# Kernel optimization log

Measured on AMD Instinct MI355X. Metric: run time of the kernel, lower is better.

The kernel has to match this reference:

```python
import jax, jax.numpy as jnp
import numpy as np

B, C, H_LEVELS = 262144, 128, 4
LEVEL_SIZES = [8, 24, 40, 56]  # partitions the C classes across hierarchy levels
ALPHA_BCE = 1.0
ALPHA_LAM = 0.5
LOG_CLAMP = -100.0  # torch F.binary_cross_entropy clamps log terms at -100


def setup_inputs() -> dict:
    key = jax.random.key(0)
    k1, k2 = jax.random.split(key)
    y_pred = jax.random.normal(k1, (B, C), dtype=jnp.float32)
    y_true = jnp.round(jax.random.uniform(k2, (B, C), dtype=jnp.float32))  # binary labels
    # La[l, c] = 1 if class c belongs to hierarchy level l (contiguous blocks)
    La = np.zeros((H_LEVELS, C), dtype=np.float32)
    off = 0
    for l, s in enumerate(LEVEL_SIZES):
        La[l, off:off + s] = 1.0
        off += s
    La = jnp.asarray(La)
    hc = jnp.arange(H_LEVELS, 0, -1).astype(jnp.float32)  # [h, h-1, ..., 1]
    lam = jnp.exp(-ALPHA_LAM * hc)
    return {"y_pred": y_pred, "y_true": y_true, "La": La, "lam": lam}


def reference(y_pred, y_true, La, lam):
    # alpha_c = alpha_d = alpha_e = 0, so only the layered-BCE term contributes.
    p = jax.nn.sigmoid(y_pred)                 # [B, C]
    pm = p[:, None, :] * La[None, :, :]        # [B, h, C] masked probs
    tm = y_true[:, None, :] * La[None, :, :]   # [B, h, C] masked targets
    log_p = jnp.clip(jnp.log(pm), LOG_CLAMP)
    log_1mp = jnp.clip(jnp.log1p(-pm), LOG_CLAMP)
    bce = -(tm * log_p + (1.0 - tm) * log_1mp)  # [B, h, C]
    per_layer = bce.mean(axis=2)                # [B, h] (mean reduction over C)
    # sum over layers weighted by lam, then sum over batch (original does NOT divide by B)
    bce_loss = jnp.sum(per_layer * lam[None, :])
    return ALPHA_BCE * bce_loss
```

## Files before the change

### kernel.cpp

```cpp
#include <hip/hip_runtime.h>

#define NCLS 128
#define HLVL 4
#define BLOCKS 8192
#define CHUNK 1024

typedef float v4f __attribute__((ext_vector_type(4)));

__global__ void prep_kernel(const float* __restrict__ La,
                            const float* __restrict__ lam,
                            float* __restrict__ w) {
    int c = threadIdx.x;
    if (c < NCLS) {
        float acc = 0.f;
#pragma unroll
        for (int l = 0; l < HLVL; ++l) acc += La[l * NCLS + c] * lam[l];
        w[c] = acc * (1.0f / (float)NCLS);
    }
}

__global__ __launch_bounds__(256) void loss_kernel(const v4f* __restrict__ yp,
                                                   const v4f* __restrict__ yt,
                                                   const float* __restrict__ w,
                                                   float* __restrict__ partial) {
    const float LOG2E = 1.44269504088896340736f;
    const float LN2   = 0.69314718055994530942f;

    int t = threadIdx.x;
    int b = blockIdx.x * CHUNK + t;
    int cbase = (t * 4) & (NCLS - 1);
    v4f w4 = *(const v4f*)(w + cbase);
    float wv[4] = {w4.x, w4.y, w4.z, w4.w};
    float wl[4] = {w4.x * LN2, w4.y * LN2, w4.z * LN2, w4.w * LN2};

    v4f x[4], y[4];
#pragma unroll
    for (int k = 0; k < 4; ++k) {
        x[k] = yp[b + k * 256];
        y[k] = yt[b + k * 256];
    }

    float acc[4] = {0.f, 0.f, 0.f, 0.f};
#pragma unroll
    for (int k = 0; k < 4; ++k) {
        float xs[4] = {x[k].x, x[k].y, x[k].z, x[k].w};
        float ts[4] = {y[k].x, y[k].y, y[k].z, y[k].w};
#pragma unroll
        for (int j = 0; j < 4; ++j) {
            float xv = xs[j];
            float e  = __builtin_amdgcn_exp2f(-fabsf(xv) * LOG2E);
            float l2 = __builtin_amdgcn_logf(1.0f + e);
            float r  = fmaf(-ts[j], xv, fmaxf(xv, 0.f));
            acc[j] = fmaf(l2, wl[j], acc[j]);
            acc[j] = fmaf(r, wv[j], acc[j]);
        }
    }
    float a = (acc[0] + acc[1]) + (acc[2] + acc[3]);

#pragma unroll
    for (int off = 32; off > 0; off >>= 1)
        a += __shfl_down(a, off, 64);

    __shared__ float bsum[4];
    if ((t & 63) == 0) bsum[t >> 6] = a;
    __syncthreads();
    if (t == 0)
        partial[blockIdx.x] = (bsum[0] + bsum[1]) + (bsum[2] + bsum[3]);
}

__global__ __launch_bounds__(256) void final_kernel(const float* __restrict__ partial,
                                                    float* __restrict__ out) {
    int t = threadIdx.x;
    float a = 0.f;
#pragma unroll
    for (int k = 0; k < BLOCKS / 256; ++k)
        a += partial[t + k * 256];
#pragma unroll
    for (int off = 32; off > 0; off >>= 1)
        a += __shfl_down(a, off, 64);
    __shared__ float bsum[4];
    if ((t & 63) == 0) bsum[t >> 6] = a;
    __syncthreads();
    if (t == 0)
        out[0] = (bsum[0] + bsum[1]) + (bsum[2] + bsum[3]);
}

extern "C" void kernel_launch(void* const* d_in, const int* in_sizes, int n_in,
                              void* d_out, int out_size, void* d_ws, size_t ws_size,
                              hipStream_t stream) {
    const float* y_pred = (const float*)d_in[0];
    const float* y_true = (const float*)d_in[1];
    const float* La     = (const float*)d_in[2];
    const float* lam    = (const float*)d_in[3];
    float* out = (float*)d_out;
    float* w       = (float*)d_ws;
    float* partial = (float*)d_ws + NCLS;

    prep_kernel<<<1, 128, 0, stream>>>(La, lam, w);

    loss_kernel<<<BLOCKS, 256, 0, stream>>>((const v4f*)y_pred,
                                            (const v4f*)y_true,
                                            w, partial);

    final_kernel<<<1, 256, 0, stream>>>(partial, out);
}
```

Baseline: 279.3 us.

## Double-buffer loss inputs through LDS with async global_load_lds pipelining

The loss kernel now has each block process a larger batch chunk in stages. Each stage's inputs are staged into a double-buffered LDS array with global_load_lds, and the next stage's copy is issued before computing on the current one. A hand-encoded s_waitcnt on vmcnt waits for the right loads. The aim is to keep more memory traffic in flight per wave and hide HBM latency, while using four times fewer blocks. In exchange the hand-written waitcnt encoding adds correctness risk and there is no lgkm wait guarding buffer reuse, and fewer blocks mean less parallelism across the GPU.

```diff
diff --git a/kernel.cpp b/kernel.cpp
--- a/kernel.cpp
+++ b/kernel.cpp
@@ -2,10 +2,15 @@
 
 #define NCLS 128
 #define HLVL 4
-#define BLOCKS 8192
-#define CHUNK 1024
+#define BLOCKS 2048
+#define BCHUNK 4096
+#define STAGE 512
+#define NSTAGE (BCHUNK / STAGE)
 
-typedef float v4f __attribute__((ext_vector_type(4)));
+typedef const __attribute__((address_space(1))) void* gas_t;
+typedef __attribute__((address_space(3))) void* las_t;
+
+#define WCNT(n) __builtin_amdgcn_s_waitcnt(((n) & 15) | 0x70 | 0xF00 | (((n) >> 4) << 14))
 
 __global__ void prep_kernel(const float* __restrict__ La,
                             const float* __restrict__ lam,
@@ -19,41 +24,61 @@
     }
 }
 
-__global__ __launch_bounds__(256) void loss_kernel(const v4f* __restrict__ yp,
-                                                   const v4f* __restrict__ yt,
+__global__ __launch_bounds__(256) void loss_kernel(const float4* __restrict__ yp,
+                                                   const float4* __restrict__ yt,
                                                    const float* __restrict__ w,
                                                    float* __restrict__ partial) {
+    __shared__ float4 lds[2][2][STAGE];
     const float LOG2E = 1.44269504088896340736f;
     const float LN2   = 0.69314718055994530942f;
 
     int t = threadIdx.x;
-    int b = blockIdx.x * CHUNK + t;
+    int wbase = t & ~63;
+    long gbase = (long)blockIdx.x * BCHUNK;
+
     int cbase = (t * 4) & (NCLS - 1);
-    v4f w4 = *(const v4f*)(w + cbase);
+    float4 w4 = *(const float4*)(w + cbase);
     float wv[4] = {w4.x, w4.y, w4.z, w4.w};
     float wl[4] = {w4.x * LN2, w4.y * LN2, w4.z * LN2, w4.w * LN2};
 
-    v4f x[4], y[4];
+    auto issue = [&](int s) {
+        int buf = s & 1;
 #pragma unroll
-    for (int k = 0; k < 4; ++k) {
-        x[k] = yp[b + k * 256];
-        y[k] = yt[b + k * 256];
-    }
+        for (int r = 0; r < 2; ++r) {
+            const float4* g0 = yp + gbase + s * STAGE + r * 256 + t;
+            const float4* g1 = yt + gbase + s * STAGE + r * 256 + t;
+            __builtin_amdgcn_global_load_lds((gas_t)g0,
+                (las_t)&lds[buf][0][r * 256 + wbase], 16, 0, 0);
+            __builtin_amdgcn_global_load_lds((gas_t)g1,
+                (las_t)&lds[buf][1][r * 256 + wbase], 16, 0, 0);
+        }
+    };
 
     float acc[4] = {0.f, 0.f, 0.f, 0.f};
+    issue(0);
 #pragma unroll
-    for (int k = 0; k < 4; ++k) {
-        float xs[4] = {x[k].x, x[k].y, x[k].z, x[k].w};
-        float ts[4] = {y[k].x, y[k].y, y[k].z, y[k].w};
+    for (int s = 0; s < NSTAGE; ++s) {
+        if (s + 1 < NSTAGE) { issue(s + 1); WCNT(4); }
+        else                { WCNT(0); }
+        __asm__ volatile("" ::: "memory");
+        int buf = s & 1;
 #pragma unroll
-        for (int j = 0; j < 4; ++j) {
-            float xv = xs[j];
-            float e  = __builtin_amdgcn_exp2f(-fabsf(xv) * LOG2E);
-            float l2 = __builtin_amdgcn_logf(1.0f + e);
-            float r  = fmaf(-ts[j], xv, fmaxf(xv, 0.f));
-            acc[j] = fmaf(l2, wl[j], acc[j]);
-            acc[j] = fmaf(r, wv[j], acc[j]);
+        for (int r = 0; r < 2; ++r) {
+            float4 x4 = lds[buf][0][r * 256 + t];
+            float4 t4 = lds[buf][1][r * 256 + t];
+            float xs[4] = {x4.x, x4.y, x4.z, x4.w};
+            float ts[4] = {t4.x, t4.y, t4.z, t4.w};
+#pragma unroll
+            for (int j = 0; j < 4; ++j) {
+                float xv = xs[j];
+                float e  = __builtin_amdgcn_exp2f(-fabsf(xv) * LOG2E);
+                float l2 = __builtin_amdgcn_logf(1.0f + e);
+                float rr = fmaf(-ts[j], xv, fmaxf(xv, 0.f));
+                acc[j] = fmaf(l2, wl[j], acc[j]);
+                acc[j] = fmaf(rr, wv[j], acc[j]);
+            }
         }
+        __asm__ volatile("" ::: "memory");
     }
     float a = (acc[0] + acc[1]) + (acc[2] + acc[3]);
 
@@ -98,8 +123,8 @@
 
     prep_kernel<<<1, 128, 0, stream>>>(La, lam, w);
 
-    loss_kernel<<<BLOCKS, 256, 0, stream>>>((const v4f*)y_pred,
-                                            (const v4f*)y_true,
+    loss_kernel<<<BLOCKS, 256, 0, stream>>>((const float4*)y_pred,
+                                            (const float4*)y_true,
                                             w, partial);
 
     final_kernel<<<1, 256, 0, stream>>>(partial, out);
```

Result: slower. 285.1 us (+2.1%).
